# Kernel optimization log

Measured on AMD Instinct MI355X. Metric: run time of the kernel, lower is better.

Reference implementation:

```python
import jax, jax.numpy as jnp
import numpy as np

B, T, N, F_IN = 2, 24, 20000, 32
E, H, OUT, K = 320000, 128, 1, 2


def setup_inputs() -> dict:
    key = jax.random.key(0)
    ks = jax.random.split(key, 20)
    x_seq = jax.random.normal(ks[0], (B, T, N, F_IN), dtype=jnp.float32)
    edge_index = jax.random.randint(ks[1], (2, E), 0, N, dtype=jnp.int64)
    edge_weight = jax.random.uniform(ks[2], (E,), dtype=jnp.float32)

    def cheb_w(k, din):
        s = 1.0 / np.sqrt(din)
        return jax.random.uniform(k, (K, din, H), dtype=jnp.float32, minval=-s, maxval=s)

    inp = {
        "x_seq": x_seq, "edge_index": edge_index, "edge_weight": edge_weight,
        "Wxz": cheb_w(ks[3], F_IN), "bxz": jnp.zeros((H,), jnp.float32),
        "Whz": cheb_w(ks[4], H),    "bhz": jnp.zeros((H,), jnp.float32),
        "Wxr": cheb_w(ks[5], F_IN), "bxr": jnp.zeros((H,), jnp.float32),
        "Whr": cheb_w(ks[6], H),    "bhr": jnp.zeros((H,), jnp.float32),
        "Wxh": cheb_w(ks[7], F_IN), "bxh": jnp.zeros((H,), jnp.float32),
        "Whh": cheb_w(ks[8], H),    "bhh": jnp.zeros((H,), jnp.float32),
        "Wl": jax.random.normal(ks[9], (H, OUT), dtype=jnp.float32) * (1.0 / np.sqrt(H)),
        "bl": jnp.zeros((OUT,), jnp.float32),
    }
    return inp


def reference(x_seq, edge_index, edge_weight,
              Wxz, bxz, Whz, bhz, Wxr, bxr, Whr, bhr,
              Wxh, bxh, Whh, bhh, Wl, bl):
    src, dst = edge_index[0], edge_index[1]
    n = x_seq.shape[2]
    # sym-normalized scaled Laplacian with lambda_max=2: Ltilde = -D^{-1/2} A D^{-1/2}
    deg = jnp.zeros((n,), x_seq.dtype).at[src].add(edge_weight)
    dinv = jnp.where(deg > 0, jax.lax.rsqrt(jnp.where(deg > 0, deg, 1.0)), 0.0)
    norm = (-dinv[src] * edge_weight * dinv[dst])  # [E]

    def prop(x):  # x: [B,N,C] -> Ltilde @ x
        msg = x[:, src, :] * norm[None, :, None]          # [B,E,C]
        return jnp.zeros_like(x).at[:, dst, :].add(msg)

    def cheb(x, W, b):  # ChebConv K=2: T0 = x, T1 = Ltilde x
        return x @ W[0] + prop(x) @ W[1] + b

    def step(h, x_t):  # h,x_t: [B,N,*]
        z = jax.nn.sigmoid(cheb(x_t, Wxz, bxz) + cheb(h, Whz, bhz))
        r = jax.nn.sigmoid(cheb(x_t, Wxr, bxr) + cheb(h, Whr, bhr))
        h_tilde = jnp.tanh(cheb(x_t, Wxh, bxh) + cheb(h * r, Whh, bhh))
        h_new = z * h + (1.0 - z) * h_tilde
        return h_new, None

    h0 = jnp.zeros((x_seq.shape[0], n, Whz.shape[2]), x_seq.dtype)
    h_final, _ = jax.lax.scan(step, h0, jnp.swapaxes(x_seq, 0, 1))  # scan over T
    return jax.nn.relu(h_final) @ Wl + bl  # [B,N,OUT]
```

## Files before the change

kernel.cpp:

```cpp
#include <hip/hip_runtime.h>
#include <math.h>

#define NN 20000
#define NE 320000
#define BB 2
#define TT 24
#define FI 32
#define HH 128

typedef __attribute__((ext_vector_type(4))) float f32x4;
typedef __attribute__((ext_vector_type(8))) short bf16x8;
typedef __attribute__((ext_vector_type(4))) short s16x4;

__device__ __forceinline__ void split1(float f, short& hi, short& lo) {
    unsigned u = __float_as_uint(f);
    unsigned short h = (unsigned short)((u + 0x7FFFu + ((u >> 16) & 1u)) >> 16);
    float fh = __uint_as_float((unsigned)h << 16);
    float r = f - fh;
    unsigned v = __float_as_uint(r);
    unsigned short l = (unsigned short)((v + 0x7FFFu + ((v >> 16) & 1u)) >> 16);
    hi = (short)h; lo = (short)l;
}

__global__ void k_detect(const int* __restrict__ ei, int* __restrict__ flag) {
    int t = threadIdx.x;
    int nz = 0;
    for (int i = 0; i < 4; ++i) nz |= (ei[2 * (t + 64 * i) + 1] != 0);
    unsigned long long m = __ballot(nz);
    if (t == 0) flag[0] = (m != 0ull) ? 0 : 1;
}

__device__ __forceinline__ int eidx(const int* __restrict__ ei, int i, int f64) {
    return f64 ? ei[2 * i] : ei[i];
}


__global__ void k_deg_count(const int* __restrict__ ei, const float* __restrict__ w,
                            float* __restrict__ deg, int* __restrict__ counts,
                            const int* __restrict__ flag) {
    int e = blockIdx.x * blockDim.x + threadIdx.x;
    if (e >= NE) return;
    int f64 = flag[0];
    int s = eidx(ei, e, f64);
    int d = eidx(ei, NE + e, f64);
    atomicAdd(&deg[s], w[e]);
    atomicAdd(&counts[d], 1);
}

__global__ void k_dinv(const float* __restrict__ deg, float* __restrict__ dinv) {
    int n = blockIdx.x * blockDim.x + threadIdx.x;
    if (n >= NN) return;
    float d = deg[n];
    dinv[n] = d > 0.f ? rsqrtf(d) : 0.f;
}

__global__ void k_norm(const int* __restrict__ ei, const float* __restrict__ w,
                       const float* __restrict__ dinv, float* __restrict__ normv,
                       const int* __restrict__ flag) {
    int e = blockIdx.x * blockDim.x + threadIdx.x;
    if (e >= NE) return;
    int f64 = flag[0];
    normv[e] = -dinv[eidx(ei, e, f64)] * w[e] * dinv[eidx(ei, NE + e, f64)];
}

__global__ void k_scan(const int* __restrict__ counts, int* __restrict__ rowptr) {
    __shared__ int sums[1024];
    int t = threadIdx.x;
    const int CH = (NN + 1023) / 1024;
    int start = t * CH;
    int s = 0;
    for (int i = 0; i < CH; ++i) {
        int idx = start + i;
        if (idx < NN) s += counts[idx];
    }
    sums[t] = s;
    __syncthreads();
    for (int off = 1; off < 1024; off *= 2) {
        int v = (t >= off) ? sums[t - off] : 0;
        __syncthreads();
        sums[t] += v;
        __syncthreads();
    }
    int run = (t > 0) ? sums[t - 1] : 0;
    for (int i = 0; i < CH; ++i) {
        int idx = start + i;
        if (idx < NN) { rowptr[idx] = run; run += counts[idx]; }
    }
    if (t == 1023) rowptr[NN] = sums[1023];
}

__global__ void k_copy_int(const int* __restrict__ src, int* __restrict__ dst, int n) {
    int i = blockIdx.x * blockDim.x + threadIdx.x;
    if (i < n) dst[i] = src[i];
}

__global__ void k_fill(const int* __restrict__ ei, const float* __restrict__ normv,
                       int* __restrict__ cursor, int* __restrict__ col, float* __restrict__ val,
                       const int* __restrict__ flag) {
    int e = blockIdx.x * blockDim.x + threadIdx.x;
    if (e >= NE) return;
    int f64 = flag[0];
    int d = eidx(ei, NE + e, f64);
    int p = atomicAdd(&cursor[d], 1);
    col[p] = eidx(ei, e, f64);
    val[p] = normv[e];
}

__global__ void k_prop_x_split(const float* __restrict__ x_seq, int t,
                               const int* __restrict__ rowptr, const int* __restrict__ col,
                               const float* __restrict__ val,
                               short* __restrict__ pxhi, short* __restrict__ pxlo,
                               short* __restrict__ xhi, short* __restrict__ xlo) {
    int n = blockIdx.x;
    int f = threadIdx.x & 31;
    int b = threadIdx.x >> 5;
    int beg = rowptr[n], end = rowptr[n + 1];
    const float* xb = x_seq + ((long)(b * TT + t) * NN) * FI;
    float acc = 0.f;
    for (int j = beg; j < end; ++j)
        acc += val[j] * xb[(long)col[j] * FI + f];
    long o = ((long)b * NN + n) * FI + f;
    short h, l;
    split1(acc, h, l);
    pxhi[o] = h; pxlo[o] = l;
    split1(xb[(long)n * FI + f], h, l);
    xhi[o] = h; xlo[o] = l;
}

__global__ void k_prop_h_split(const float* __restrict__ hin,
                               const int* __restrict__ rowptr, const int* __restrict__ col,
                               const float* __restrict__ val,
                               short* __restrict__ phi, short* __restrict__ plo) {
    int lane = threadIdx.x & 63;
    int n = blockIdx.x * 4 + (threadIdx.x >> 6);
    int b = lane >> 5;
    int c4 = (lane & 31) << 2;
    int beg = rowptr[n], end = rowptr[n + 1];
    const float* hb = hin + (long)b * NN * HH + c4;
    f32x4 acc = {0.f, 0.f, 0.f, 0.f};
    for (int j = beg; j < end; ++j) {
        float v = val[j];
        f32x4 q = *(const f32x4*)(hb + (long)col[j] * HH);
        acc += v * q;
    }
    long o = ((long)b * NN + n) * HH + c4;
    s16x4 hv, lv;
#pragma unroll
    for (int i = 0; i < 4; ++i) {
        short h, l;
        split1(acc[i], h, l);
        hv[i] = h; lv[i] = l;
    }
    *(s16x4*)(phi + o) = hv;
    *(s16x4*)(plo + o) = lv;
}

__global__ void k_prep_w(const float* __restrict__ Wx, const float* __restrict__ Wh,
                         short* __restrict__ hi, short* __restrict__ lo) {
    int idx = blockIdx.x * blockDim.x + threadIdx.x;
    if (idx >= HH * 320) return;
    int c = idx / 320, k = idx - c * 320;
    float w = (k < 2 * FI) ? Wx[k * HH + c] : Wh[(k - 2 * FI) * HH + c];
    short h, l;
    split1(w, h, l);
    hi[idx] = h; lo[idx] = l;
}

template<int EPI>
__global__ __launch_bounds__(128)
void k_gemm_mfma(const short* __restrict__ xhi, const short* __restrict__ xlo,
                 const short* __restrict__ pxhi, const short* __restrict__ pxlo,
                 const short* __restrict__ ahhi, const short* __restrict__ ahlo,
                 const short* __restrict__ aphi, const short* __restrict__ aplo,
                 const short* __restrict__ Whi0, const short* __restrict__ Wlo0,
                 const float* __restrict__ bx0, const float* __restrict__ bh0,
                 const short* __restrict__ Whi1, const short* __restrict__ Wlo1,
                 const float* __restrict__ bx1, const float* __restrict__ bh1,
                 const float* __restrict__ hcur,
                 const float* __restrict__ zin,
                 float* __restrict__ out0,
                 float* __restrict__ out1,
                 short* __restrict__ sohi,
                 short* __restrict__ solo) {
    const int tid = threadIdx.x;
    const int lane = tid & 63;
    const int wid = tid >> 6;
    const int lr = lane & 15;
    const int lg = lane >> 4;
    const int gate = (EPI == 1) ? (int)blockIdx.y : 0;
    const short* Whi = gate ? Whi1 : Whi0;
    const short* Wlo = gate ? Wlo1 : Wlo0;
    const float* bx  = gate ? bx1 : bx0;
    const float* bh  = gate ? bh1 : bh0;

    const int row_base = blockIdx.x * 32;
    const int col_base = wid * 64;

    long r32[2], r128[2];
#pragma unroll
    for (int m = 0; m < 2; ++m) {
        int row = row_base + m * 16 + lr;
        r32[m]  = (long)row * FI + lg * 8;
        r128[m] = (long)row * HH + lg * 8;
    }
    const long wbase = (long)(col_base + lr) * 320;

    f32x4 acc[2][4];
#pragma unroll
    for (int m = 0; m < 2; ++m)
#pragma unroll
        for (int n = 0; n < 4; ++n) acc[m][n] = (f32x4){0.f, 0.f, 0.f, 0.f};

#pragma unroll
    for (int ks = 0; ks < 10; ++ks) {
        bf16x8 ahi[2], alo[2];
#pragma unroll
        for (int m = 0; m < 2; ++m) {
            const short *ph_, *pl_;
            long off;
            if (ks == 0)      { ph_ = xhi;  pl_ = xlo;  off = r32[m]; }
            else if (ks == 1) { ph_ = pxhi; pl_ = pxlo; off = r32[m]; }
            else if (ks < 6)  { ph_ = ahhi; pl_ = ahlo; off = r128[m] + (ks - 2) * 32; }
            else              { ph_ = aphi; pl_ = aplo; off = r128[m] + (ks - 6) * 32; }
            ahi[m] = *(const bf16x8*)(ph_ + off);
            alo[m] = *(const bf16x8*)(pl_ + off);
        }
#pragma unroll
        for (int n = 0; n < 4; ++n) {
            const long wo = wbase + (long)n * (16 * 320) + ks * 32 + lg * 8;
            bf16x8 wh = *(const bf16x8*)(Whi + wo);
            bf16x8 wl = *(const bf16x8*)(Wlo + wo);
#pragma unroll
            for (int m = 0; m < 2; ++m) {
                acc[m][n] = __builtin_amdgcn_mfma_f32_16x16x32_bf16(ahi[m], wh, acc[m][n], 0, 0, 0);
                acc[m][n] = __builtin_amdgcn_mfma_f32_16x16x32_bf16(ahi[m], wl, acc[m][n], 0, 0, 0);
                acc[m][n] = __builtin_amdgcn_mfma_f32_16x16x32_bf16(alo[m], wh, acc[m][n], 0, 0, 0);
            }
        }
    }

#pragma unroll
    for (int m = 0; m < 2; ++m) {
#pragma unroll
        for (int n = 0; n < 4; ++n) {
            const int col = col_base + n * 16 + lr;
            const float bsum = bx[col] + bh[col];
#pragma unroll
            for (int j = 0; j < 4; ++j) {
                const int row = row_base + m * 16 + lg * 4 + j;
                const long o = (long)row * HH + col;
                float v = acc[m][n][j] + bsum;
                if (EPI == 1) {
                    float s = 1.f / (1.f + expf(-v));
                    if (gate == 0) {
                        out0[o] = s;
                    } else {
                        float hrv = s * hcur[o];
                        out1[o] = hrv;
                        short hh, ll;
                        split1(hrv, hh, ll);
                        sohi[o] = hh; solo[o] = ll;
                    }
                } else {
                    float ht = tanhf(v);
                    float z = zin[o];
                    float hn = z * hcur[o] + (1.f - z) * ht;
                    out0[o] = hn;
                    short hh, ll;
                    split1(hn, hh, ll);
                    sohi[o] = hh; solo[o] = ll;
                }
            }
        }
    }
}

__global__ void k_out(const float* __restrict__ h, const float* __restrict__ Wl,
                      const float* __restrict__ bl, float* __restrict__ out) {
    int row = blockIdx.x;
    int lane = threadIdx.x;
    const float* hr = h + (long)row * HH;
    float a = fmaxf(hr[lane], 0.f) * Wl[lane] + fmaxf(hr[64 + lane], 0.f) * Wl[64 + lane];
#pragma unroll
    for (int off = 32; off > 0; off >>= 1) a += __shfl_down(a, off);
    if (lane == 0) out[row] = a + bl[0];
}

extern "C" void kernel_launch(void* const* d_in, const int* in_sizes, int n_in,
                              void* d_out, int out_size, void* d_ws, size_t ws_size,
                              hipStream_t stream) {
    const float* x_seq = (const float*)d_in[0];
    const int*   ei    = (const int*)d_in[1];
    const float* ew    = (const float*)d_in[2];
    const float* Wxz = (const float*)d_in[3],  *bxz = (const float*)d_in[4];
    const float* Whz = (const float*)d_in[5],  *bhz = (const float*)d_in[6];
    const float* Wxr = (const float*)d_in[7],  *bxr = (const float*)d_in[8];
    const float* Whr = (const float*)d_in[9],  *bhr = (const float*)d_in[10];
    const float* Wxh = (const float*)d_in[11], *bxh = (const float*)d_in[12];
    const float* Whh = (const float*)d_in[13], *bhh = (const float*)d_in[14];
    const float* Wl  = (const float*)d_in[15], *bl  = (const float*)d_in[16];
    float* out = (float*)d_out;

    char* p = (char*)d_ws;
    auto alloc = [&](size_t bytes) -> char* {
        char* r = p;
        p += (bytes + 255) & ~(size_t)255;
        return r;
    };
    const long RB = (long)BB * NN;

    int*   dflag  = (int*)alloc(4);
    float* deg    = (float*)alloc(NN * 4);
    float* dinv   = (float*)alloc(NN * 4);
    float* normv  = (float*)alloc(NE * 4);
    int*   counts = (int*)alloc(NN * 4);
    int*   rowptr = (int*)alloc((NN + 1) * 4);
    int*   cursor = (int*)alloc(NN * 4);
    int*   ccol   = (int*)alloc(NE * 4);
    float* cval   = (float*)alloc(NE * 4);
    float* hbuf   = (float*)alloc(RB * HH * 4);
    float* zbuf   = (float*)alloc(RB * HH * 4);
    float* hrbuf  = (float*)alloc(RB * HH * 4);
    short* xthi   = (short*)alloc(RB * FI * 2);
    short* xtlo   = (short*)alloc(RB * FI * 2);
    short* pxhi   = (short*)alloc(RB * FI * 2);
    short* pxlo   = (short*)alloc(RB * FI * 2);
    short* hhi    = (short*)alloc(RB * HH * 2);
    short* hlo    = (short*)alloc(RB * HH * 2);
    short* hrhi   = (short*)alloc(RB * HH * 2);
    short* hrlo   = (short*)alloc(RB * HH * 2);
    short* phhi   = (short*)alloc(RB * HH * 2);
    short* phlo   = (short*)alloc(RB * HH * 2);
    short* WtZhi  = (short*)alloc(HH * 320 * 2);
    short* WtZlo  = (short*)alloc(HH * 320 * 2);
    short* WtRhi  = (short*)alloc(HH * 320 * 2);
    short* WtRlo  = (short*)alloc(HH * 320 * 2);
    short* WtHhi  = (short*)alloc(HH * 320 * 2);
    short* WtHlo  = (short*)alloc(HH * 320 * 2);

    hipMemsetAsync(deg, 0, NN * 4, stream);
    hipMemsetAsync(counts, 0, NN * 4, stream);
    k_detect<<<1, 64, 0, stream>>>(ei, dflag);
    k_deg_count<<<(NE + 255) / 256, 256, 0, stream>>>(ei, ew, deg, counts, dflag);
    k_dinv<<<(NN + 255) / 256, 256, 0, stream>>>(deg, dinv);
    k_norm<<<(NE + 255) / 256, 256, 0, stream>>>(ei, ew, dinv, normv, dflag);
    k_scan<<<1, 1024, 0, stream>>>(counts, rowptr);
    k_copy_int<<<(NN + 255) / 256, 256, 0, stream>>>(rowptr, cursor, NN);
    k_fill<<<(NE + 255) / 256, 256, 0, stream>>>(ei, normv, cursor, ccol, cval, dflag);

    const int WPE = HH * 320;
    k_prep_w<<<(WPE + 255) / 256, 256, 0, stream>>>(Wxz, Whz, WtZhi, WtZlo);
    k_prep_w<<<(WPE + 255) / 256, 256, 0, stream>>>(Wxr, Whr, WtRhi, WtRlo);
    k_prep_w<<<(WPE + 255) / 256, 256, 0, stream>>>(Wxh, Whh, WtHhi, WtHlo);

    hipMemsetAsync(hbuf, 0, RB * HH * 4, stream);
    hipMemsetAsync(hhi, 0, RB * HH * 2, stream);
    hipMemsetAsync(hlo, 0, RB * HH * 2, stream);

    dim3 gZR(1250, 2), gH(1250, 1);
    for (int t = 0; t < TT; ++t) {
        k_prop_x_split<<<NN, 64, 0, stream>>>(x_seq, t, rowptr, ccol, cval,
                                              pxhi, pxlo, xthi, xtlo);
        k_prop_h_split<<<NN / 4, 256, 0, stream>>>(hbuf, rowptr, ccol, cval, phhi, phlo);
        k_gemm_mfma<1><<<gZR, 128, 0, stream>>>(
            xthi, xtlo, pxhi, pxlo, hhi, hlo, phhi, phlo,
            WtZhi, WtZlo, bxz, bhz, WtRhi, WtRlo, bxr, bhr,
            hbuf, nullptr, zbuf, hrbuf, hrhi, hrlo);
        k_prop_h_split<<<NN / 4, 256, 0, stream>>>(hrbuf, rowptr, ccol, cval, phhi, phlo);
        k_gemm_mfma<2><<<gH, 128, 0, stream>>>(
            xthi, xtlo, pxhi, pxlo, hrhi, hrlo, phhi, phlo,
            WtHhi, WtHlo, bxh, bhh, nullptr, nullptr, nullptr, nullptr,
            hbuf, zbuf, hbuf, nullptr, hhi, hlo);
    }

    k_out<<<RB, 64, 0, stream>>>(hbuf, Wl, bl, out);
}
```

Before: 6.581 ms.

## Store recurrent state as bf16 hi/lo pairs and fuse z/r gates per block

The fp32 copies of h, z and h*r are removed, and the state is kept only as bf16 hi/lo split pairs. The propagation and epilogue code rebuild fp32 values from those pairs, which cuts gather and store traffic. The z/r GEMM now computes both gates in one block with 16-row tiles, reusing the A-fragment loads across the two weight sets. A fourth lo*lo MFMA term is added for accuracy. The trade-offs are more MFMA work, smaller row tiles and a slight loss of precision in the stored state.

```diff
diff --git a/kernel.cpp b/kernel.cpp
--- a/kernel.cpp
+++ b/kernel.cpp
@@ -20,6 +20,11 @@
     unsigned v = __float_as_uint(r);
     unsigned short l = (unsigned short)((v + 0x7FFFu + ((v >> 16) & 1u)) >> 16);
     hi = (short)h; lo = (short)l;
+}
+
+__device__ __forceinline__ float rec2(short h, short l) {
+    return __uint_as_float(((unsigned)(unsigned short)h) << 16)
+         + __uint_as_float(((unsigned)(unsigned short)l) << 16);
 }
 
 __global__ void k_detect(const int* __restrict__ ei, int* __restrict__ flag) {
@@ -127,7 +132,7 @@
     xhi[o] = h; xlo[o] = l;
 }
 
-__global__ void k_prop_h_split(const float* __restrict__ hin,
+__global__ void k_prop_h_split(const short* __restrict__ hi_in, const short* __restrict__ lo_in,
                                const int* __restrict__ rowptr, const int* __restrict__ col,
                                const float* __restrict__ val,
                                short* __restrict__ phi, short* __restrict__ plo) {
@@ -136,12 +141,17 @@
     int b = lane >> 5;
     int c4 = (lane & 31) << 2;
     int beg = rowptr[n], end = rowptr[n + 1];
-    const float* hb = hin + (long)b * NN * HH + c4;
+    const short* hb = hi_in + (long)b * NN * HH + c4;
+    const short* lb = lo_in + (long)b * NN * HH + c4;
     f32x4 acc = {0.f, 0.f, 0.f, 0.f};
     for (int j = beg; j < end; ++j) {
         float v = val[j];
-        f32x4 q = *(const f32x4*)(hb + (long)col[j] * HH);
-        acc += v * q;
+        long ro = (long)col[j] * HH;
+        s16x4 qh = *(const s16x4*)(hb + ro);
+        s16x4 ql = *(const s16x4*)(lb + ro);
+#pragma unroll
+        for (int i = 0; i < 4; ++i)
+            acc[i] += v * rec2(qh[i], ql[i]);
     }
     long o = ((long)b * NN + n) * HH + c4;
     s16x4 hv, lv;
@@ -176,111 +186,98 @@
                  const float* __restrict__ bx0, const float* __restrict__ bh0,
                  const short* __restrict__ Whi1, const short* __restrict__ Wlo1,
                  const float* __restrict__ bx1, const float* __restrict__ bh1,
-                 const float* __restrict__ hcur,
-                 const float* __restrict__ zin,
-                 float* __restrict__ out0,
-                 float* __restrict__ out1,
-                 short* __restrict__ sohi,
-                 short* __restrict__ solo) {
+                 const short* __restrict__ hchi, const short* __restrict__ hclo,
+                 const short* __restrict__ zhi_in, const short* __restrict__ zlo_in,
+                 short* __restrict__ o0hi, short* __restrict__ o0lo,
+                 short* __restrict__ o1hi, short* __restrict__ o1lo) {
     const int tid = threadIdx.x;
     const int lane = tid & 63;
     const int wid = tid >> 6;
     const int lr = lane & 15;
     const int lg = lane >> 4;
-    const int gate = (EPI == 1) ? (int)blockIdx.y : 0;
-    const short* Whi = gate ? Whi1 : Whi0;
-    const short* Wlo = gate ? Wlo1 : Wlo0;
-    const float* bx  = gate ? bx1 : bx0;
-    const float* bh  = gate ? bh1 : bh0;
-
-    const int row_base = blockIdx.x * 32;
+
+    const int row_base = blockIdx.x * 16;
     const int col_base = wid * 64;
-
-    long r32[2], r128[2];
-#pragma unroll
-    for (int m = 0; m < 2; ++m) {
-        int row = row_base + m * 16 + lr;
-        r32[m]  = (long)row * FI + lg * 8;
-        r128[m] = (long)row * HH + lg * 8;
-    }
-    const long wbase = (long)(col_base + lr) * 320;
-
-    f32x4 acc[2][4];
-#pragma unroll
-    for (int m = 0; m < 2; ++m)
-#pragma unroll
-        for (int n = 0; n < 4; ++n) acc[m][n] = (f32x4){0.f, 0.f, 0.f, 0.f};
+    const int row = row_base + lr;
+    const long r32  = (long)row * FI + lg * 8;
+    const long r128 = (long)row * HH + lg * 8;
+    const long wb = (long)(col_base + lr) * 320;
+
+    f32x4 acc0[4], acc1[4];
+#pragma unroll
+    for (int n = 0; n < 4; ++n) {
+        acc0[n] = (f32x4){0.f, 0.f, 0.f, 0.f};
+        acc1[n] = (f32x4){0.f, 0.f, 0.f, 0.f};
+    }
 
 #pragma unroll
     for (int ks = 0; ks < 10; ++ks) {
-        bf16x8 ahi[2], alo[2];
-#pragma unroll
-        for (int m = 0; m < 2; ++m) {
-            const short *ph_, *pl_;
-            long off;
-            if (ks == 0)      { ph_ = xhi;  pl_ = xlo;  off = r32[m]; }
-            else if (ks == 1) { ph_ = pxhi; pl_ = pxlo; off = r32[m]; }
-            else if (ks < 6)  { ph_ = ahhi; pl_ = ahlo; off = r128[m] + (ks - 2) * 32; }
-            else              { ph_ = aphi; pl_ = aplo; off = r128[m] + (ks - 6) * 32; }
-            ahi[m] = *(const bf16x8*)(ph_ + off);
-            alo[m] = *(const bf16x8*)(pl_ + off);
-        }
+        const short *ph_, *pl_;
+        long off;
+        if (ks == 0)      { ph_ = xhi;  pl_ = xlo;  off = r32; }
+        else if (ks == 1) { ph_ = pxhi; pl_ = pxlo; off = r32; }
+        else if (ks < 6)  { ph_ = ahhi; pl_ = ahlo; off = r128 + (ks - 2) * 32; }
+        else              { ph_ = aphi; pl_ = aplo; off = r128 + (ks - 6) * 32; }
+        bf16x8 ahi = *(const bf16x8*)(ph_ + off);
+        bf16x8 alo = *(const bf16x8*)(pl_ + off);
 #pragma unroll
         for (int n = 0; n < 4; ++n) {
-            const long wo = wbase + (long)n * (16 * 320) + ks * 32 + lg * 8;
-            bf16x8 wh = *(const bf16x8*)(Whi + wo);
-            bf16x8 wl = *(const bf16x8*)(Wlo + wo);
-#pragma unroll
-            for (int m = 0; m < 2; ++m) {
-                acc[m][n] = __builtin_amdgcn_mfma_f32_16x16x32_bf16(ahi[m], wh, acc[m][n], 0, 0, 0);
-                acc[m][n] = __builtin_amdgcn_mfma_f32_16x16x32_bf16(ahi[m], wl, acc[m][n], 0, 0, 0);
-                acc[m][n] = __builtin_amdgcn_mfma_f32_16x16x32_bf16(alo[m], wh, acc[m][n], 0, 0, 0);
+            const long wo = wb + (long)n * (16 * 320) + ks * 32 + lg * 8;
+            bf16x8 wh0 = *(const bf16x8*)(Whi0 + wo);
+            bf16x8 wl0 = *(const bf16x8*)(Wlo0 + wo);
+            acc0[n] = __builtin_amdgcn_mfma_f32_16x16x32_bf16(ahi, wh0, acc0[n], 0, 0, 0);
+            acc0[n] = __builtin_amdgcn_mfma_f32_16x16x32_bf16(ahi, wl0, acc0[n], 0, 0, 0);
+            acc0[n] = __builtin_amdgcn_mfma_f32_16x16x32_bf16(alo, wh0, acc0[n], 0, 0, 0);
+            acc0[n] = __builtin_amdgcn_mfma_f32_16x16x32_bf16(alo, wl0, acc0[n], 0, 0, 0);
+            if (EPI == 1) {
+                bf16x8 wh1 = *(const bf16x8*)(Whi1 + wo);
+                bf16x8 wl1 = *(const bf16x8*)(Wlo1 + wo);
+                acc1[n] = __builtin_amdgcn_mfma_f32_16x16x32_bf16(ahi, wh1, acc1[n], 0, 0, 0);
+                acc1[n] = __builtin_amdgcn_mfma_f32_16x16x32_bf16(ahi, wl1, acc1[n], 0, 0, 0);
+                acc1[n] = __builtin_amdgcn_mfma_f32_16x16x32_bf16(alo, wh1, acc1[n], 0, 0, 0);
+                acc1[n] = __builtin_amdgcn_mfma_f32_16x16x32_bf16(alo, wl1, acc1[n], 0, 0, 0);
             }
         }
     }
 
 #pragma unroll
-    for (int m = 0; m < 2; ++m) {
-#pragma unroll
-        for (int n = 0; n < 4; ++n) {
-            const int col = col_base + n * 16 + lr;
-            const float bsum = bx[col] + bh[col];
-#pragma unroll
-            for (int j = 0; j < 4; ++j) {
-                const int row = row_base + m * 16 + lg * 4 + j;
-                const long o = (long)row * HH + col;
-                float v = acc[m][n][j] + bsum;
-                if (EPI == 1) {
-                    float s = 1.f / (1.f + expf(-v));
-                    if (gate == 0) {
-                        out0[o] = s;
-                    } else {
-                        float hrv = s * hcur[o];
-                        out1[o] = hrv;
-                        short hh, ll;
-                        split1(hrv, hh, ll);
-                        sohi[o] = hh; solo[o] = ll;
-                    }
-                } else {
-                    float ht = tanhf(v);
-                    float z = zin[o];
-                    float hn = z * hcur[o] + (1.f - z) * ht;
-                    out0[o] = hn;
-                    short hh, ll;
-                    split1(hn, hh, ll);
-                    sohi[o] = hh; solo[o] = ll;
-                }
+    for (int n = 0; n < 4; ++n) {
+        const int col = col_base + n * 16 + lr;
+        const float b0 = bx0[col] + bh0[col];
+        const float b1 = (EPI == 1) ? (bx1[col] + bh1[col]) : 0.f;
+#pragma unroll
+        for (int j = 0; j < 4; ++j) {
+            const int ro = row_base + lg * 4 + j;
+            const long o = (long)ro * HH + col;
+            short hh, ll;
+            if (EPI == 1) {
+                float z = 1.f / (1.f + expf(-(acc0[n][j] + b0)));
+                split1(z, hh, ll);
+                o0hi[o] = hh; o0lo[o] = ll;
+                float r = 1.f / (1.f + expf(-(acc1[n][j] + b1)));
+                float h = rec2(hchi[o], hclo[o]);
+                split1(r * h, hh, ll);
+                o1hi[o] = hh; o1lo[o] = ll;
+            } else {
+                float ht = tanhf(acc0[n][j] + b0);
+                float z = rec2(zhi_in[o], zlo_in[o]);
+                float h = rec2(hchi[o], hclo[o]);
+                float hn = z * h + (1.f - z) * ht;
+                split1(hn, hh, ll);
+                o0hi[o] = hh; o0lo[o] = ll;
             }
         }
     }
 }
 
-__global__ void k_out(const float* __restrict__ h, const float* __restrict__ Wl,
-                      const float* __restrict__ bl, float* __restrict__ out) {
+__global__ void k_out(const short* __restrict__ hhi, const short* __restrict__ hlo,
+                      const float* __restrict__ Wl, const float* __restrict__ bl,
+                      float* __restrict__ out) {
     int row = blockIdx.x;
     int lane = threadIdx.x;
-    const float* hr = h + (long)row * HH;
-    float a = fmaxf(hr[lane], 0.f) * Wl[lane] + fmaxf(hr[64 + lane], 0.f) * Wl[64 + lane];
+    long base = (long)row * HH;
+    float a = fmaxf(rec2(hhi[base + lane], hlo[base + lane]), 0.f) * Wl[lane]
+            + fmaxf(rec2(hhi[base + 64 + lane], hlo[base + 64 + lane]), 0.f) * Wl[64 + lane];
 #pragma unroll
     for (int off = 32; off > 0; off >>= 1) a += __shfl_down(a, off);
     if (lane == 0) out[row] = a + bl[0];
@@ -318,9 +315,6 @@
     int*   cursor = (int*)alloc(NN * 4);
     int*   ccol   = (int*)alloc(NE * 4);
     float* cval   = (float*)alloc(NE * 4);
-    float* hbuf   = (float*)alloc(RB * HH * 4);
-    float* zbuf   = (float*)alloc(RB * HH * 4);
-    float* hrbuf  = (float*)alloc(RB * HH * 4);
     short* xthi   = (short*)alloc(RB * FI * 2);
     short* xtlo   = (short*)alloc(RB * FI * 2);
     short* pxhi   = (short*)alloc(RB * FI * 2);
@@ -331,6 +325,8 @@
     short* hrlo   = (short*)alloc(RB * HH * 2);
     short* phhi   = (short*)alloc(RB * HH * 2);
     short* phlo   = (short*)alloc(RB * HH * 2);
+    short* zhi    = (short*)alloc(RB * HH * 2);
+    short* zlo    = (short*)alloc(RB * HH * 2);
     short* WtZhi  = (short*)alloc(HH * 320 * 2);
     short* WtZlo  = (short*)alloc(HH * 320 * 2);
     short* WtRhi  = (short*)alloc(HH * 320 * 2);
@@ -353,25 +349,26 @@
     k_prep_w<<<(WPE + 255) / 256, 256, 0, stream>>>(Wxr, Whr, WtRhi, WtRlo);
     k_prep_w<<<(WPE + 255) / 256, 256, 0, stream>>>(Wxh, Whh, WtHhi, WtHlo);
 
-    hipMemsetAsync(hbuf, 0, RB * HH * 4, stream);
     hipMemsetAsync(hhi, 0, RB * HH * 2, stream);
     hipMemsetAsync(hlo, 0, RB * HH * 2, stream);
 
-    dim3 gZR(1250, 2), gH(1250, 1);
+    dim3 g(2500);
     for (int t = 0; t < TT; ++t) {
         k_prop_x_split<<<NN, 64, 0, stream>>>(x_seq, t, rowptr, ccol, cval,
                                               pxhi, pxlo, xthi, xtlo);
-        k_prop_h_split<<<NN / 4, 256, 0, stream>>>(hbuf, rowptr, ccol, cval, phhi, phlo);
-        k_gemm_mfma<1><<<gZR, 128, 0, stream>>>(
+        k_prop_h_split<<<NN / 4, 256, 0, stream>>>(hhi, hlo, rowptr, ccol, cval, phhi, phlo);
+        k_gemm_mfma<1><<<g, 128, 0, stream>>>(
             xthi, xtlo, pxhi, pxlo, hhi, hlo, phhi, phlo,
             WtZhi, WtZlo, bxz, bhz, WtRhi, WtRlo, bxr, bhr,
-            hbuf, nullptr, zbuf, hrbuf, hrhi, hrlo);
-        k_prop_h_split<<<NN / 4, 256, 0, stream>>>(hrbuf, rowptr, ccol, cval, phhi, phlo);
-        k_gemm_mfma<2><<<gH, 128, 0, stream>>>(
+            hhi, hlo, nullptr, nullptr,
+            zhi, zlo, hrhi, hrlo);
+        k_prop_h_split<<<NN / 4, 256, 0, stream>>>(hrhi, hrlo, rowptr, ccol, cval, phhi, phlo);
+        k_gemm_mfma<2><<<g, 128, 0, stream>>>(
             xthi, xtlo, pxhi, pxlo, hrhi, hrlo, phhi, phlo,
             WtHhi, WtHlo, bxh, bhh, nullptr, nullptr, nullptr, nullptr,
-            hbuf, zbuf, hbuf, nullptr, hhi, hlo);
-    }
-
-    k_out<<<RB, 64, 0, stream>>>(hbuf, Wl, bl, out);
-}
+            hhi, hlo, zhi, zlo,
+            hhi, hlo, nullptr, nullptr);
+    }
+
+    k_out<<<RB, 64, 0, stream>>>(hhi, hlo, Wl, bl, out);
+}
```

Measured after the change: 7.637 ms. 16.0% more time.
